# Performance work log

Measured on AMD Instinct MI355X. Metric: run time of the kernel, lower is better.

Reference implementation:

```python
import jax, jax.numpy as jnp
import numpy as np

N, D, H, K, E, C = 50000, 128, 128, 5, 800000, 1


def _xavier(key, shape):
    fan_in, fan_out = shape[-2], shape[-1]
    a = (6.0 / (fan_in + fan_out)) ** 0.5
    return jax.random.uniform(key, shape, jnp.float32, -a, a)


def setup_inputs() -> dict:
    key = jax.random.key(0)
    ks = jax.random.split(key, 16)
    inp = {
        "x": jax.random.normal(ks[0], (N, D), jnp.float32),
        "edge_index_A1": jax.random.randint(ks[1], (2, E), 0, N),
        "edge_index_A2": jax.random.randint(ks[2], (2, E), 0, N),
        "edge_index_A3": jax.random.randint(ks[3], (2, E), 0, N),
        # rgcn1: 3 relation weights (D,H), linear (H,H)+bias
        "W1": _xavier(ks[4], (3, D, H)),
        "lin1_w": _xavier(ks[5], (H, H)),
        "lin1_b": jnp.zeros((H,), jnp.float32),
        # rgcn2
        "W2": _xavier(ks[6], (3, H, H)),
        "lin2_w": _xavier(ks[7], (H, H)),
        "lin2_b": jnp.zeros((H,), jnp.float32),
        # KAN layer
        "kan_w": _xavier(ks[8], (H, H)),
        "kan_b": jnp.zeros((H,), jnp.float32),
        "alpha": jnp.ones((H,), jnp.float32),
        "beta": jnp.zeros((H,), jnp.float32),
        "knots": jnp.linspace(-1.0, 1.0, K, dtype=jnp.float32),
        "spline_vals": jax.random.normal(ks[9], (H, K), jnp.float32),
        # final fc
        "fc_w": _xavier(ks[10], (C, H)),
        "fc_b": jnp.zeros((C,), jnp.float32),
    }
    return inp


def _rgcn(x, edges, Wr, lw, lb):
    # out[row] += (x @ W_r)[col], summed over relations, then linear
    out = jnp.zeros((x.shape[0], lw.shape[1]), x.dtype)
    for ei, W in zip(edges, Wr):  # fixed 3 relations
        msg = (x @ W)[ei[1]]  # gather transformed source feats
        out = out + jax.ops.segment_sum(msg, ei[0], num_segments=x.shape[0])
    return out @ lw.T + lb


def _natural_cubic_eval(knots, values, x):
    # knots (K,), values (F,K), x (N,F) -> (N,F)
    Kn = knots.shape[0]
    h = knots[1:] - knots[:-1]  # (K-1,)
    slope = (values[:, 1:] - values[:, :-1]) / h  # (F,K-1)
    rhs = 6.0 * (slope[:, 1:] - slope[:, :-1])  # (F,K-2)
    A = (jnp.diag(2.0 * (h[:-1] + h[1:]))
         + jnp.diag(h[1:-1], 1) + jnp.diag(h[1:-1], -1))
    M_inner = jnp.linalg.solve(A, rhs.T).T  # (F,K-2)
    M = jnp.pad(M_inner, ((0, 0), (1, 1)))  # natural BCs: M[0]=M[-1]=0
    j = jnp.clip(jnp.searchsorted(knots, x, side="right") - 1, 0, Kn - 2)
    f = jnp.arange(values.shape[0])[None, :]
    t0, t1 = knots[j], knots[j + 1]
    hj = t1 - t0
    y0, y1 = values[f, j], values[f, j + 1]
    M0, M1 = M[f, j], M[f, j + 1]
    a, b = t1 - x, x - t0
    return (M0 * a ** 3 / (6 * hj) + M1 * b ** 3 / (6 * hj)
            + (y0 / hj - M0 * hj / 6) * a + (y1 / hj - M1 * hj / 6) * b)


def reference(x, edge_index_A1, edge_index_A2, edge_index_A3,
              W1, lin1_w, lin1_b, W2, lin2_w, lin2_b,
              kan_w, kan_b, alpha, beta, knots, spline_vals,
              fc_w, fc_b):
    edges = (edge_index_A1, edge_index_A2, edge_index_A3)
    h1 = jax.nn.relu(_rgcn(x, edges, W1, lin1_w, lin1_b))
    h2 = jax.nn.relu(_rgcn(h1, edges, W2, lin2_w, lin2_b))
    k = alpha * (h2 @ kan_w.T + kan_b) + beta
    k = _natural_cubic_eval(knots, spline_vals, k)
    out = k @ fc_w.T + fc_b  # (N,1)
    return jnp.squeeze(out, axis=1)
```

## Files before the change

### kernel.cpp

```cpp
#include <hip/hip_runtime.h>

#define HD 128
#define EPB 4096

typedef __attribute__((ext_vector_type(8))) short bf16x8;
typedef __attribute__((ext_vector_type(4))) float f32x4;
typedef __attribute__((ext_vector_type(4))) unsigned int u32x4;

static __device__ __forceinline__ float bf2f(unsigned short u) {
    union { unsigned int i; float f; } c; c.i = ((unsigned int)u) << 16; return c.f;
}
static __device__ __forceinline__ unsigned short f2bf(float f) {
    union { float f; unsigned int i; } c; c.f = f;
    unsigned int lsb = (c.i >> 16) & 1;
    c.i += 0x7fffu + lsb;
    return (unsigned short)(c.i >> 16);
}

__global__ void spline_solve(const float* __restrict__ knots,
                             const float* __restrict__ vals,
                             float* __restrict__ M) {
    int f = threadIdx.x;
    float kn[5], v[5];
#pragma unroll
    for (int i = 0; i < 5; ++i) { kn[i] = knots[i]; v[i] = vals[f * 5 + i]; }
    float h[4], sl[4];
#pragma unroll
    for (int i = 0; i < 4; ++i) { h[i] = kn[i + 1] - kn[i]; sl[i] = (v[i + 1] - v[i]) / h[i]; }
    float r0 = 6.f * (sl[1] - sl[0]);
    float r1 = 6.f * (sl[2] - sl[1]);
    float r2 = 6.f * (sl[3] - sl[2]);
    float d0 = 2.f * (h[0] + h[1]), d1 = 2.f * (h[1] + h[2]), d2 = 2.f * (h[2] + h[3]);
    float e0 = h[1], e1 = h[2];
    float w1 = e0 / d0;  float d1p = d1 - w1 * e0;  float r1p = r1 - w1 * r0;
    float w2 = e1 / d1p; float d2p = d2 - w2 * e1;  float r2p = r2 - w2 * r1p;
    float x2 = r2p / d2p;
    float x1 = (r1p - e1 * x2) / d1p;
    float x0 = (r0 - e0 * x1) / d0;
    M[f * 5 + 0] = 0.f; M[f * 5 + 1] = x0; M[f * 5 + 2] = x1; M[f * 5 + 3] = x2; M[f * 5 + 4] = 0.f;
}

__global__ void xcast(const float* __restrict__ x, unsigned short* __restrict__ xb) {
    long i = ((long)blockIdx.x * blockDim.x + threadIdx.x) * 8;
    float4 f0 = *(const float4*)(x + i);
    float4 f1 = *(const float4*)(x + i + 4);
    ushort4 o0, o1;
    o0.x = f2bf(f0.x); o0.y = f2bf(f0.y); o0.z = f2bf(f0.z); o0.w = f2bf(f0.w);
    o1.x = f2bf(f1.x); o1.y = f2bf(f1.y); o1.z = f2bf(f1.z); o1.w = f2bf(f1.w);
    *(ushort4*)(xb + i) = o0;
    *(ushort4*)(xb + i + 4) = o1;
}

__global__ void uprep(const float* __restrict__ W1, const float* __restrict__ W2,
                      const float* __restrict__ l1, const float* __restrict__ l2,
                      const float* __restrict__ kw, unsigned short* __restrict__ Wt) {
    int mat = blockIdx.y, c = blockIdx.x, k = threadIdx.x;
    if (mat == 6) {
        Wt[(long)6 * 16384 + c * HD + k] = f2bf(kw[c * HD + k]);
        return;
    }
    const float* Wr = (mat < 3) ? (W1 + (long)mat * 16384) : (W2 + (long)(mat - 3) * 16384);
    const float* L  = (mat < 3) ? l1 : l2;
    __shared__ float Lrow[HD];
    Lrow[k] = L[c * HD + k];
    __syncthreads();
    float s = 0.f;
#pragma unroll 8
    for (int j = 0; j < HD; ++j) s += Wr[k * HD + j] * Lrow[j];
    Wt[(long)mat * 16384 + c * HD + k] = f2bf(s);
}

template <int MODE>
__global__ __launch_bounds__(256) void mfma_gemm(
    const unsigned short* __restrict__ A, const unsigned short* __restrict__ Wt,
    void* __restrict__ Out, const float* __restrict__ bias,
    const float* __restrict__ alpha, const float* __restrict__ beta,
    const float* __restrict__ knots, const float* __restrict__ vals,
    const float* __restrict__ Msp, const float* __restrict__ fcw,
    const float* __restrict__ fcb, int n) {
    constexpr int NREL = (MODE == 1) ? 3 : 1;
    constexpr int RS   = (MODE == 1) ? 384 : 128;
    __shared__ unsigned short As[64 * HD];
    __shared__ unsigned short Ws[HD * HD];
    const int t = threadIdx.x;
    const int row0 = blockIdx.x * 64;
    const int w = t >> 6;
    const int lane = t & 63;
    const int m = lane & 15;
    const int g = lane >> 4;
    const int sw = (m & 7) << 4;

    f32x4 acc[8];
#pragma unroll
    for (int ct = 0; ct < 8; ++ct) acc[ct] = (f32x4){0.f, 0.f, 0.f, 0.f};

#pragma unroll
    for (int rel = 0; rel < NREL; ++rel) {
        if (rel) __syncthreads();
        const unsigned short* Wg = Wt + (long)rel * 16384;
        for (int i = t; i < 2048; i += 256) {
            u32x4 v = *(const u32x4*)(Wg + i * 8);
            int byte = (i * 16) ^ (((i >> 4) & 7) << 4);
            *(u32x4*)((char*)Ws + byte) = v;
        }
        for (int i = t; i < 1024; i += 256) {
            int rr = i >> 4;
            int k8 = (i & 15) << 3;
            int row = row0 + rr;
            u32x4 v = (u32x4){0u, 0u, 0u, 0u};
            if (row < n) v = *(const u32x4*)(A + (long)row * RS + rel * HD + k8);
            int byte = (i * 16) ^ ((rr & 7) << 4);
            *(u32x4*)((char*)As + byte) = v;
        }
        __syncthreads();
#pragma unroll
        for (int ks = 0; ks < 4; ++ks) {
            const int kb = ks * 64 + g * 16;
            bf16x8 af = *(const bf16x8*)((const char*)As + ((((w * 16 + m) << 8) + kb) ^ sw));
#pragma unroll
            for (int ct = 0; ct < 8; ++ct) {
                bf16x8 bf = *(const bf16x8*)((const char*)Ws + ((((ct * 16 + m) << 8) + kb) ^ sw));
                acc[ct] = __builtin_amdgcn_mfma_f32_16x16x32_bf16(af, bf, acc[ct], 0, 0, 0);
            }
        }
    }

    if (MODE == 1) {
        unsigned short* C = (unsigned short*)Out;
#pragma unroll
        for (int ct = 0; ct < 8; ++ct) {
            float bv = bias[ct * 16 + m];
#pragma unroll
            for (int r = 0; r < 4; ++r) {
                int row = row0 + w * 16 + g * 4 + r;
                if (row < n)
                    C[(long)row * HD + ct * 16 + m] = f2bf(fmaxf(acc[ct][r] + bv, 0.f));
            }
        }
    } else {
        float kn[5];
#pragma unroll
        for (int i = 0; i < 5; ++i) kn[i] = knots[i];
        float part[4] = {0.f, 0.f, 0.f, 0.f};
#pragma unroll
        for (int ct = 0; ct < 8; ++ct) {
            int f = ct * 16 + m;
            float kb = bias[f], al = alpha[f], be = beta[f], fw = fcw[f];
#pragma unroll
            for (int r = 0; r < 4; ++r) {
                float xv = al * (acc[ct][r] + kb) + be;
                int j = -1;
#pragma unroll
                for (int k = 0; k < 5; ++k) j += (xv >= kn[k]) ? 1 : 0;
                j = max(0, min(3, j));
                float t0 = kn[j], t1 = kn[j + 1];
                float hj = t1 - t0;
                float y0 = vals[f * 5 + j], y1 = vals[f * 5 + j + 1];
                float M0 = Msp[f * 5 + j], M1 = Msp[f * 5 + j + 1];
                float a = t1 - xv, b = xv - t0;
                float inv6h = 1.f / (6.f * hj);
                float s = M0 * a * a * a * inv6h + M1 * b * b * b * inv6h
                        + (y0 / hj - M0 * hj / 6.f) * a + (y1 / hj - M1 * hj / 6.f) * b;
                part[r] += s * fw;
            }
        }
#pragma unroll
        for (int o = 1; o < 16; o <<= 1) {
#pragma unroll
            for (int r = 0; r < 4; ++r) part[r] += __shfl_xor(part[r], o);
        }
        if (m == 0) {
#pragma unroll
            for (int r = 0; r < 4; ++r) {
                int row = row0 + w * 16 + g * 4 + r;
                if (row < n) ((float*)Out)[row] = part[r] + fcb[0];
            }
        }
    }
}

__global__ __launch_bounds__(256) void hist_pass(
    const int* __restrict__ e0, const int* __restrict__ e1,
    const int* __restrict__ e2, int* __restrict__ Hmat,
    int E, int NBLK, int NBUK) {
    __shared__ int hist[1024];
    const int r = blockIdx.y, blk = blockIdx.x, t = threadIdx.x;
    const int* dst = (r == 0) ? e0 : ((r == 1) ? e1 : e2);
    for (int i = t; i < NBUK; i += 256) hist[i] = 0;
    __syncthreads();
    const int s0 = blk * EPB, s1 = min(s0 + EPB, E);
    for (int e = s0 + t; e < s1; e += 256) atomicAdd(&hist[dst[e] >> 6], 1);
    __syncthreads();
    for (int b = t; b < NBUK; b += 256)
        Hmat[((long)r * NBUK + b) * NBLK + blk] = hist[b];
}

__global__ __launch_bounds__(256) void scanA(const int* __restrict__ cnt,
                                             int* __restrict__ S,
                                             int* __restrict__ bsum, int n) {
    __shared__ int ts[256];
    const int t = threadIdx.x;
    const int base = blockIdx.x * 2048 + t * 8;
    int v[8];
    int s = 0;
#pragma unroll
    for (int i = 0; i < 8; ++i) {
        int j = base + i;
        v[i] = (j < n) ? cnt[j] : 0;
        s += v[i];
    }
    ts[t] = s;
    __syncthreads();
    for (int off = 1; off < 256; off <<= 1) {
        int x = (t >= off) ? ts[t - off] : 0;
        __syncthreads();
        ts[t] += x;
        __syncthreads();
    }
    int excl = ts[t] - s;
#pragma unroll
    for (int i = 0; i < 8; ++i) {
        int j = base + i;
        if (j < n) S[j] = excl;
        excl += v[i];
    }
    if (t == 255) bsum[blockIdx.x] = ts[255];
}

__global__ __launch_bounds__(256) void scanC(int* __restrict__ S,
                                             const int* __restrict__ bsum,
                                             int n, int total) {
    __shared__ int red[256];
    const int t = threadIdx.x;
    int acc = 0;
    for (int b = t; b < blockIdx.x; b += 256) acc += bsum[b];
    red[t] = acc;
    __syncthreads();
    for (int o = 128; o; o >>= 1) {
        if (t < o) red[t] += red[t + o];
        __syncthreads();
    }
    const int off = red[0];
    const int base = blockIdx.x * 2048 + t * 8;
#pragma unroll
    for (int i = 0; i < 8; ++i) {
        int j = base + i;
        if (j < n) S[j] += off;
    }
    if (blockIdx.x == gridDim.x - 1 && t == 0) S[n] = total;
}

__global__ void bptr_fill(const int* __restrict__ O, int* __restrict__ bptr,
                          int NBLK, int nb3, int total) {
    int i = blockIdx.x * blockDim.x + threadIdx.x;
    if (i < nb3) bptr[i] = O[(long)i * NBLK];
    else if (i == nb3) bptr[i] = total;
}

__global__ __launch_bounds__(256) void fill_pass(
    const int* __restrict__ e0, const int* __restrict__ e1,
    const int* __restrict__ e2, const int* __restrict__ O,
    unsigned int* __restrict__ P, int E, int NBLK, int NBUK) {
    __shared__ int cur[1024];
    const int r = blockIdx.y, blk = blockIdx.x, t = threadIdx.x;
    const int* eb = (r == 0) ? e0 : ((r == 1) ? e1 : e2);
    for (int b = t; b < NBUK; b += 256)
        cur[b] = O[((long)r * NBUK + b) * NBLK + blk];
    __syncthreads();
    const int s0 = blk * EPB, s1 = min(s0 + EPB, E);
    for (int e = s0 + t; e < s1; e += 256) {
        int dst = eb[e], src = eb[E + e];
        int pos = atomicAdd(&cur[dst >> 6], 1);
        P[pos] = ((unsigned)(dst & 63) << 16) | (unsigned)src;
    }
}

__global__ __launch_bounds__(256) void bucket_scatter2(
    const unsigned int* __restrict__ P, const int* __restrict__ bptr,
    unsigned short* __restrict__ srcs, int* __restrict__ S,
    int N, int NBUK, int E3) {
    __shared__ int cnt[64], cur[64];
    const int b = blockIdx.x, r = blockIdx.y, t = threadIdx.x;
    const int d0 = b * 64;
    const int pb = bptr[r * NBUK + b], pe = bptr[r * NBUK + b + 1];
    if (t < 64) cnt[t] = 0;
    __syncthreads();
    for (int i = pb + t; i < pe; i += 256) atomicAdd(&cnt[P[i] >> 16], 1);
    __syncthreads();
    if (t < 64) {
        int v = cnt[t];
        int x = v;
#pragma unroll
        for (int o = 1; o < 64; o <<= 1) {
            int y = __shfl_up(x, o);
            if (t >= o) x += y;
        }
        int start = pb + x - v;
        cur[t] = start;
        int d = d0 + t;
        if (d < N) S[(long)r * N + d] = start;
    }
    __syncthreads();
    for (int i = pb + t; i < pe; i += 256) {
        unsigned pk = P[i];
        int pos = atomicAdd(&cur[pk >> 16], 1);
        srcs[pos] = (unsigned short)(pk & 0xFFFFu);
    }
    if (b == NBUK - 1 && r == 2 && t == 0) S[(long)3 * N] = E3;
}

__global__ __launch_bounds__(256) void csr_agg3(const unsigned short* __restrict__ X,
                                                const int* __restrict__ S,
                                                const unsigned short* __restrict__ srcs,
                                                unsigned short* __restrict__ Ag, int N) {
    const int g = threadIdx.x >> 5;
    const int lane = threadIdx.x & 31;
    const int d = blockIdx.x * 8 + g;
    if (d >= N) return;
    const unsigned short* Xb = X + lane * 4;
#pragma unroll
    for (int r = 0; r < 3; ++r) {
        const int beg = S[(long)r * N + d];
        const int end = S[(long)r * N + d + 1];
        float a0[4] = {0.f, 0.f, 0.f, 0.f};
        float a1[4] = {0.f, 0.f, 0.f, 0.f};
        float a2[4] = {0.f, 0.f, 0.f, 0.f};
        float a3[4] = {0.f, 0.f, 0.f, 0.f};
        int e = beg;
        for (; e + 3 < end; e += 4) {
            int s0 = srcs[e], s1 = srcs[e + 1], s2 = srcs[e + 2], s3 = srcs[e + 3];
            ushort4 u0 = *(const ushort4*)&Xb[(long)s0 * HD];
            ushort4 u1 = *(const ushort4*)&Xb[(long)s1 * HD];
            ushort4 u2 = *(const ushort4*)&Xb[(long)s2 * HD];
            ushort4 u3 = *(const ushort4*)&Xb[(long)s3 * HD];
            a0[0] += bf2f(u0.x); a0[1] += bf2f(u0.y); a0[2] += bf2f(u0.z); a0[3] += bf2f(u0.w);
            a1[0] += bf2f(u1.x); a1[1] += bf2f(u1.y); a1[2] += bf2f(u1.z); a1[3] += bf2f(u1.w);
            a2[0] += bf2f(u2.x); a2[1] += bf2f(u2.y); a2[2] += bf2f(u2.z); a2[3] += bf2f(u2.w);
            a3[0] += bf2f(u3.x); a3[1] += bf2f(u3.y); a3[2] += bf2f(u3.z); a3[3] += bf2f(u3.w);
        }
        for (; e < end; ++e) {
            ushort4 u0 = *(const ushort4*)&Xb[(long)srcs[e] * HD];
            a0[0] += bf2f(u0.x); a0[1] += bf2f(u0.y); a0[2] += bf2f(u0.z); a0[3] += bf2f(u0.w);
        }
        ushort4 o;
        o.x = f2bf((a0[0] + a1[0]) + (a2[0] + a3[0]));
        o.y = f2bf((a0[1] + a1[1]) + (a2[1] + a3[1]));
        o.z = f2bf((a0[2] + a1[2]) + (a2[2] + a3[2]));
        o.w = f2bf((a0[3] + a1[3]) + (a2[3] + a3[3]));
        *(ushort4*)&Ag[(long)d * 384 + r * HD + lane * 4] = o;
    }
}

extern "C" void kernel_launch(void* const* d_in, const int* in_sizes, int n_in,
                              void* d_out, int out_size, void* d_ws, size_t ws_size,
                              hipStream_t stream) {
    const float* x       = (const float*)d_in[0];
    const int*   eA[3]   = {(const int*)d_in[1], (const int*)d_in[2], (const int*)d_in[3]};
    const float* W1      = (const float*)d_in[4];
    const float* lin1_w  = (const float*)d_in[5];
    const float* lin1_b  = (const float*)d_in[6];
    const float* W2      = (const float*)d_in[7];
    const float* lin2_w  = (const float*)d_in[8];
    const float* lin2_b  = (const float*)d_in[9];
    const float* kan_w   = (const float*)d_in[10];
    const float* kan_b   = (const float*)d_in[11];
    const float* alpha   = (const float*)d_in[12];
    const float* beta    = (const float*)d_in[13];
    const float* knots   = (const float*)d_in[14];
    const float* spline_vals = (const float*)d_in[15];
    const float* fc_w    = (const float*)d_in[16];
    const float* fc_b    = (const float*)d_in[17];

    const int N = in_sizes[0] / HD;
    const int E = in_sizes[1] / 2;
    const int NBUK = (N + 63) / 64;
    const int NBLK = (E + EPB - 1) / EPB;
    const int nH   = 3 * NBUK * NBLK;
    const int nb3  = 3 * NBUK;

    char* p = (char*)d_ws;
    auto carve = [&](size_t bytes) {
        char* q = p;
        p += (bytes + 255) & ~(size_t)255;
        return q;
    };
    float* M              = (float*)carve(4096);
    unsigned short* Wt    = (unsigned short*)carve((size_t)7 * 16384 * 2);
    int* Hmat             = (int*)carve((size_t)nH * 4);
    int* O                = (int*)carve((size_t)(nH + 1) * 4);
    int* bsum             = (int*)carve(4096);
    int* bptr             = (int*)carve((size_t)(nb3 + 1) * 4);
    int* S                = (int*)carve((size_t)(3 * N + 1) * 4);
    unsigned int* P       = (unsigned int*)carve((size_t)3 * E * 4);
    unsigned short* srcs  = (unsigned short*)carve((size_t)3 * E * 2);
    unsigned short* xb    = (unsigned short*)carve((size_t)N * HD * 2);
    unsigned short* hb    = (unsigned short*)carve((size_t)N * HD * 2);
    unsigned short* Ag    = (unsigned short*)carve((size_t)N * 384 * 2);

    const int g64      = (N + 63) / 64;
    const int aggGrid  = (N + 7) / 8;
    const int scanGrid = (nH + 2047) / 2048;

    spline_solve<<<1, 128, 0, stream>>>(knots, spline_vals, M);
    xcast<<<(N * HD) / (256 * 8), 256, 0, stream>>>(x, xb);
    uprep<<<dim3(128, 7), 128, 0, stream>>>(W1, W2, lin1_w, lin2_w, kan_w, Wt);

    hist_pass<<<dim3(NBLK, 3), 256, 0, stream>>>(eA[0], eA[1], eA[2], Hmat, E, NBLK, NBUK);
    scanA<<<scanGrid, 256, 0, stream>>>(Hmat, O, bsum, nH);
    scanC<<<scanGrid, 256, 0, stream>>>(O, bsum, nH, 3 * E);
    bptr_fill<<<(nb3 + 256) / 256, 256, 0, stream>>>(O, bptr, NBLK, nb3, 3 * E);
    fill_pass<<<dim3(NBLK, 3), 256, 0, stream>>>(eA[0], eA[1], eA[2], O, P, E, NBLK, NBUK);
    bucket_scatter2<<<dim3(NBUK, 3), 256, 0, stream>>>(P, bptr, srcs, S, N, NBUK, 3 * E);

    csr_agg3<<<aggGrid, 256, 0, stream>>>(xb, S, srcs, Ag, N);
    mfma_gemm<1><<<g64, 256, 0, stream>>>(Ag, Wt, hb, lin1_b, nullptr, nullptr,
                                          nullptr, nullptr, nullptr, nullptr, nullptr, N);

    csr_agg3<<<aggGrid, 256, 0, stream>>>(hb, S, srcs, Ag, N);
    mfma_gemm<1><<<g64, 256, 0, stream>>>(Ag, Wt + (size_t)3 * 16384, hb, lin2_b, nullptr,
                                          nullptr, nullptr, nullptr, nullptr, nullptr, nullptr, N);

    mfma_gemm<2><<<g64, 256, 0, stream>>>(hb, Wt + (size_t)6 * 16384, d_out, kan_b, alpha,
                                          beta, knots, spline_vals, M, fc_w, fc_b, N);
}
```

Measured before the change: 336.5 us.

## Merge prep kernels, widen sort buckets to 256 nodes, drop bptr_fill

Fuses the spline solve, weight precompute and x bf16 cast into one launch. Widens the destination buckets in the two-level counting sort from 64 to 256 nodes, so the histogram and offset matrices shrink by four and the scan gets cheaper. Bucket bounds are now read straight from the offset matrix, which removes the bptr_fill launch. The cost is a 256-wide shared-memory scan in bucket_scatter2 with many syncthreads, more atomic contention per bucket, and an implicit limit of NBUK ≤ 256.

New measurement: 317.9 us. 5.5% less time.

```diff
diff --git a/kernel.cpp b/kernel.cpp
--- a/kernel.cpp
+++ b/kernel.cpp
@@ -2,6 +2,7 @@
 
 #define HD 128
 #define EPB 4096
+#define BUK 256
 
 typedef __attribute__((ext_vector_type(8))) short bf16x8;
 typedef __attribute__((ext_vector_type(4))) float f32x4;
@@ -17,57 +18,68 @@
     return (unsigned short)(c.i >> 16);
 }
 
-__global__ void spline_solve(const float* __restrict__ knots,
-                             const float* __restrict__ vals,
-                             float* __restrict__ M) {
-    int f = threadIdx.x;
-    float kn[5], v[5];
-#pragma unroll
-    for (int i = 0; i < 5; ++i) { kn[i] = knots[i]; v[i] = vals[f * 5 + i]; }
-    float h[4], sl[4];
-#pragma unroll
-    for (int i = 0; i < 4; ++i) { h[i] = kn[i + 1] - kn[i]; sl[i] = (v[i + 1] - v[i]) / h[i]; }
-    float r0 = 6.f * (sl[1] - sl[0]);
-    float r1 = 6.f * (sl[2] - sl[1]);
-    float r2 = 6.f * (sl[3] - sl[2]);
-    float d0 = 2.f * (h[0] + h[1]), d1 = 2.f * (h[1] + h[2]), d2 = 2.f * (h[2] + h[3]);
-    float e0 = h[1], e1 = h[2];
-    float w1 = e0 / d0;  float d1p = d1 - w1 * e0;  float r1p = r1 - w1 * r0;
-    float w2 = e1 / d1p; float d2p = d2 - w2 * e1;  float r2p = r2 - w2 * r1p;
-    float x2 = r2p / d2p;
-    float x1 = (r1p - e1 * x2) / d1p;
-    float x0 = (r0 - e0 * x1) / d0;
-    M[f * 5 + 0] = 0.f; M[f * 5 + 1] = x0; M[f * 5 + 2] = x1; M[f * 5 + 3] = x2; M[f * 5 + 4] = 0.f;
-}
-
-__global__ void xcast(const float* __restrict__ x, unsigned short* __restrict__ xb) {
-    long i = ((long)blockIdx.x * blockDim.x + threadIdx.x) * 8;
-    float4 f0 = *(const float4*)(x + i);
-    float4 f1 = *(const float4*)(x + i + 4);
-    ushort4 o0, o1;
-    o0.x = f2bf(f0.x); o0.y = f2bf(f0.y); o0.z = f2bf(f0.z); o0.w = f2bf(f0.w);
-    o1.x = f2bf(f1.x); o1.y = f2bf(f1.y); o1.z = f2bf(f1.z); o1.w = f2bf(f1.w);
-    *(ushort4*)(xb + i) = o0;
-    *(ushort4*)(xb + i + 4) = o1;
-}
-
-__global__ void uprep(const float* __restrict__ W1, const float* __restrict__ W2,
-                      const float* __restrict__ l1, const float* __restrict__ l2,
-                      const float* __restrict__ kw, unsigned short* __restrict__ Wt) {
-    int mat = blockIdx.y, c = blockIdx.x, k = threadIdx.x;
-    if (mat == 6) {
-        Wt[(long)6 * 16384 + c * HD + k] = f2bf(kw[c * HD + k]);
+__global__ __launch_bounds__(256) void prep(
+    const float* __restrict__ knots, const float* __restrict__ vals,
+    float* __restrict__ M,
+    const float* __restrict__ W1, const float* __restrict__ W2,
+    const float* __restrict__ l1, const float* __restrict__ l2,
+    const float* __restrict__ kw, unsigned short* __restrict__ Wt,
+    const float* __restrict__ x, unsigned short* __restrict__ xb, long nxh) {
+    const int bid = blockIdx.x;
+    const int t = threadIdx.x;
+    if (bid == 0) {
+        if (t < 128) {
+            int f = t;
+            float kn[5], v[5];
+#pragma unroll
+            for (int i = 0; i < 5; ++i) { kn[i] = knots[i]; v[i] = vals[f * 5 + i]; }
+            float h[4], sl[4];
+#pragma unroll
+            for (int i = 0; i < 4; ++i) { h[i] = kn[i+1] - kn[i]; sl[i] = (v[i+1] - v[i]) / h[i]; }
+            float r0 = 6.f * (sl[1] - sl[0]);
+            float r1 = 6.f * (sl[2] - sl[1]);
+            float r2 = 6.f * (sl[3] - sl[2]);
+            float d0 = 2.f * (h[0] + h[1]), d1 = 2.f * (h[1] + h[2]), d2 = 2.f * (h[2] + h[3]);
+            float e0 = h[1], e1 = h[2];
+            float w1 = e0 / d0;  float d1p = d1 - w1 * e0;  float r1p = r1 - w1 * r0;
+            float w2 = e1 / d1p; float d2p = d2 - w2 * e1;  float r2p = r2 - w2 * r1p;
+            float x2 = r2p / d2p;
+            float x1 = (r1p - e1 * x2) / d1p;
+            float x0 = (r0 - e0 * x1) / d0;
+            M[f*5+0] = 0.f; M[f*5+1] = x0; M[f*5+2] = x1; M[f*5+3] = x2; M[f*5+4] = 0.f;
+        }
         return;
     }
-    const float* Wr = (mat < 3) ? (W1 + (long)mat * 16384) : (W2 + (long)(mat - 3) * 16384);
-    const float* L  = (mat < 3) ? l1 : l2;
-    __shared__ float Lrow[HD];
-    Lrow[k] = L[c * HD + k];
-    __syncthreads();
-    float s = 0.f;
+    if (bid < 897) {
+        __shared__ float Lrow[HD];
+        const int id = bid - 1;
+        const int mat = id >> 7, c = id & 127;
+        if (mat == 6) {
+            if (t < 128) Wt[(long)6 * 16384 + c * HD + t] = f2bf(kw[c * HD + t]);
+            return;
+        }
+        const float* Wr = (mat < 3) ? (W1 + (long)mat * 16384) : (W2 + (long)(mat - 3) * 16384);
+        const float* L  = (mat < 3) ? l1 : l2;
+        if (t < 128) Lrow[t] = L[c * HD + t];
+        __syncthreads();
+        if (t < 128) {
+            float s = 0.f;
 #pragma unroll 8
-    for (int j = 0; j < HD; ++j) s += Wr[k * HD + j] * Lrow[j];
-    Wt[(long)mat * 16384 + c * HD + k] = f2bf(s);
+            for (int j = 0; j < HD; ++j) s += Wr[t * HD + j] * Lrow[j];
+            Wt[(long)mat * 16384 + c * HD + t] = f2bf(s);
+        }
+        return;
+    }
+    long i = ((long)(bid - 897) * 256 + t) * 8;
+    if (i < nxh) {
+        float4 f0 = *(const float4*)(x + i);
+        float4 f1 = *(const float4*)(x + i + 4);
+        ushort4 o0, o1;
+        o0.x = f2bf(f0.x); o0.y = f2bf(f0.y); o0.z = f2bf(f0.z); o0.w = f2bf(f0.w);
+        o1.x = f2bf(f1.x); o1.y = f2bf(f1.y); o1.z = f2bf(f1.z); o1.w = f2bf(f1.w);
+        *(ushort4*)(xb + i) = o0;
+        *(ushort4*)(xb + i + 4) = o1;
+    }
 }
 
 template <int MODE>
@@ -183,16 +195,15 @@
     const int* __restrict__ e0, const int* __restrict__ e1,
     const int* __restrict__ e2, int* __restrict__ Hmat,
     int E, int NBLK, int NBUK) {
-    __shared__ int hist[1024];
+    __shared__ int hist[256];
     const int r = blockIdx.y, blk = blockIdx.x, t = threadIdx.x;
     const int* dst = (r == 0) ? e0 : ((r == 1) ? e1 : e2);
-    for (int i = t; i < NBUK; i += 256) hist[i] = 0;
+    if (t < NBUK) hist[t] = 0;
     __syncthreads();
     const int s0 = blk * EPB, s1 = min(s0 + EPB, E);
-    for (int e = s0 + t; e < s1; e += 256) atomicAdd(&hist[dst[e] >> 6], 1);
-    __syncthreads();
-    for (int b = t; b < NBUK; b += 256)
-        Hmat[((long)r * NBUK + b) * NBLK + blk] = hist[b];
+    for (int e = s0 + t; e < s1; e += 256) atomicAdd(&hist[dst[e] >> 8], 1);
+    __syncthreads();
+    if (t < NBUK) Hmat[((long)r * NBUK + t) * NBLK + blk] = hist[t];
 }
 
 __global__ __launch_bounds__(256) void scanA(const int* __restrict__ cnt,
@@ -250,61 +261,55 @@
     if (blockIdx.x == gridDim.x - 1 && t == 0) S[n] = total;
 }
 
-__global__ void bptr_fill(const int* __restrict__ O, int* __restrict__ bptr,
-                          int NBLK, int nb3, int total) {
-    int i = blockIdx.x * blockDim.x + threadIdx.x;
-    if (i < nb3) bptr[i] = O[(long)i * NBLK];
-    else if (i == nb3) bptr[i] = total;
-}
-
 __global__ __launch_bounds__(256) void fill_pass(
     const int* __restrict__ e0, const int* __restrict__ e1,
     const int* __restrict__ e2, const int* __restrict__ O,
     unsigned int* __restrict__ P, int E, int NBLK, int NBUK) {
-    __shared__ int cur[1024];
+    __shared__ int cur[256];
     const int r = blockIdx.y, blk = blockIdx.x, t = threadIdx.x;
     const int* eb = (r == 0) ? e0 : ((r == 1) ? e1 : e2);
-    for (int b = t; b < NBUK; b += 256)
-        cur[b] = O[((long)r * NBUK + b) * NBLK + blk];
+    if (t < NBUK) cur[t] = O[((long)r * NBUK + t) * NBLK + blk];
     __syncthreads();
     const int s0 = blk * EPB, s1 = min(s0 + EPB, E);
     for (int e = s0 + t; e < s1; e += 256) {
         int dst = eb[e], src = eb[E + e];
-        int pos = atomicAdd(&cur[dst >> 6], 1);
-        P[pos] = ((unsigned)(dst & 63) << 16) | (unsigned)src;
+        int pos = atomicAdd(&cur[dst >> 8], 1);
+        P[pos] = ((unsigned)(dst & 255) << 16) | (unsigned)src;
     }
 }
 
 __global__ __launch_bounds__(256) void bucket_scatter2(
-    const unsigned int* __restrict__ P, const int* __restrict__ bptr,
+    const unsigned int* __restrict__ P, const int* __restrict__ O,
     unsigned short* __restrict__ srcs, int* __restrict__ S,
-    int N, int NBUK, int E3) {
-    __shared__ int cnt[64], cur[64];
+    int N, int NBUK, int NBLK, int E3) {
+    __shared__ int cnt[256], pos[256], cur[256];
     const int b = blockIdx.x, r = blockIdx.y, t = threadIdx.x;
-    const int d0 = b * 64;
-    const int pb = bptr[r * NBUK + b], pe = bptr[r * NBUK + b + 1];
-    if (t < 64) cnt[t] = 0;
+    const int d0 = b * BUK;
+    const long oidx = (long)r * NBUK + b;
+    const int pb = O[oidx * NBLK];
+    const int pe = (oidx + 1 < (long)3 * NBUK) ? O[(oidx + 1) * NBLK] : E3;
+    cnt[t] = 0;
     __syncthreads();
     for (int i = pb + t; i < pe; i += 256) atomicAdd(&cnt[P[i] >> 16], 1);
     __syncthreads();
-    if (t < 64) {
-        int v = cnt[t];
-        int x = v;
-#pragma unroll
-        for (int o = 1; o < 64; o <<= 1) {
-            int y = __shfl_up(x, o);
-            if (t >= o) x += y;
-        }
-        int start = pb + x - v;
-        cur[t] = start;
-        int d = d0 + t;
-        if (d < N) S[(long)r * N + d] = start;
-    }
+    int v = cnt[t];
+    pos[t] = v;
+    __syncthreads();
+    for (int off = 1; off < 256; off <<= 1) {
+        int x = (t >= off) ? pos[t - off] : 0;
+        __syncthreads();
+        pos[t] += x;
+        __syncthreads();
+    }
+    int start = pb + pos[t] - v;
+    cur[t] = start;
+    int d = d0 + t;
+    if (d < N) S[(long)r * N + d] = start;
     __syncthreads();
     for (int i = pb + t; i < pe; i += 256) {
         unsigned pk = P[i];
-        int pos = atomicAdd(&cur[pk >> 16], 1);
-        srcs[pos] = (unsigned short)(pk & 0xFFFFu);
+        int p2 = atomicAdd(&cur[pk >> 16], 1);
+        srcs[p2] = (unsigned short)(pk & 0xFFFFu);
     }
     if (b == NBUK - 1 && r == 2 && t == 0) S[(long)3 * N] = E3;
 }
@@ -373,10 +378,9 @@
 
     const int N = in_sizes[0] / HD;
     const int E = in_sizes[1] / 2;
-    const int NBUK = (N + 63) / 64;
+    const int NBUK = (N + BUK - 1) / BUK;
     const int NBLK = (E + EPB - 1) / EPB;
     const int nH   = 3 * NBUK * NBLK;
-    const int nb3  = 3 * NBUK;
 
     char* p = (char*)d_ws;
     auto carve = [&](size_t bytes) {
@@ -389,7 +393,6 @@
     int* Hmat             = (int*)carve((size_t)nH * 4);
     int* O                = (int*)carve((size_t)(nH + 1) * 4);
     int* bsum             = (int*)carve(4096);
-    int* bptr             = (int*)carve((size_t)(nb3 + 1) * 4);
     int* S                = (int*)carve((size_t)(3 * N + 1) * 4);
     unsigned int* P       = (unsigned int*)carve((size_t)3 * E * 4);
     unsigned short* srcs  = (unsigned short*)carve((size_t)3 * E * 2);
@@ -397,20 +400,21 @@
     unsigned short* hb    = (unsigned short*)carve((size_t)N * HD * 2);
     unsigned short* Ag    = (unsigned short*)carve((size_t)N * 384 * 2);
 
+    const long nxh = (long)N * HD;
+    const int xcastB = (int)((nxh + 2047) / 2048);
+    const int prepGrid = 1 + 896 + xcastB;
     const int g64      = (N + 63) / 64;
     const int aggGrid  = (N + 7) / 8;
     const int scanGrid = (nH + 2047) / 2048;
 
-    spline_solve<<<1, 128, 0, stream>>>(knots, spline_vals, M);
-    xcast<<<(N * HD) / (256 * 8), 256, 0, stream>>>(x, xb);
-    uprep<<<dim3(128, 7), 128, 0, stream>>>(W1, W2, lin1_w, lin2_w, kan_w, Wt);
+    prep<<<prepGrid, 256, 0, stream>>>(knots, spline_vals, M, W1, W2, lin1_w, lin2_w,
+                                       kan_w, Wt, x, xb, nxh);
 
     hist_pass<<<dim3(NBLK, 3), 256, 0, stream>>>(eA[0], eA[1], eA[2], Hmat, E, NBLK, NBUK);
     scanA<<<scanGrid, 256, 0, stream>>>(Hmat, O, bsum, nH);
     scanC<<<scanGrid, 256, 0, stream>>>(O, bsum, nH, 3 * E);
-    bptr_fill<<<(nb3 + 256) / 256, 256, 0, stream>>>(O, bptr, NBLK, nb3, 3 * E);
     fill_pass<<<dim3(NBLK, 3), 256, 0, stream>>>(eA[0], eA[1], eA[2], O, P, E, NBLK, NBUK);
-    bucket_scatter2<<<dim3(NBUK, 3), 256, 0, stream>>>(P, bptr, srcs, S, N, NBUK, 3 * E);
+    bucket_scatter2<<<dim3(NBUK, 3), 256, 0, stream>>>(P, O, srcs, S, N, NBUK, NBLK, 3 * E);
 
     csr_agg3<<<aggGrid, 256, 0, stream>>>(xb, S, srcs, Ag, N);
     mfma_gemm<1><<<g64, 256, 0, stream>>>(Ag, Wt, hb, lin1_b, nullptr, nullptr,
```
